# Performance work log

Measured on AMD Instinct MI355X. Metric: run time of the kernel, lower is better.

## Reference

```python
import jax, jax.numpy as jnp
import numpy as np

D = 256          # common_dim = specific_dim
NH = 8           # num_heads
HD = D // NH     # head_dim = 32
B, S = 16, 1024
EPS = 1e-5


def _mha(q, k, v, wq, bq, wk, bk, wv, bv, wo, bo):
    # q,k,v: [B, S, D]; weights stored [in, out] so y = x @ w + b
    b_, _, _ = q.shape

    def proj(x, w, b):
        return (x @ w + b).reshape(b_, -1, NH, HD).transpose(0, 2, 1, 3)  # [B,H,S,hd]

    Q, K, V = proj(q, wq, bq), proj(k, wk, bk), proj(v, wv, bv)
    scores = jnp.einsum('bhqd,bhkd->bhqk', Q, K) / (float(HD) ** 0.5)
    attn = jax.nn.softmax(scores, axis=-1)
    out = jnp.einsum('bhqk,bhkd->bhqd', attn, V)
    out = out.transpose(0, 2, 1, 3).reshape(b_, -1, D)
    return out @ wo + bo


def _ln(x, g, b):
    mu = jnp.mean(x, axis=-1, keepdims=True)
    var = jnp.var(x, axis=-1, keepdims=True)
    return (x - mu) * jax.lax.rsqrt(var + EPS) * g + b


def setup_inputs() -> dict:
    key = jax.random.key(0)
    ks = iter(jax.random.split(key, 32))
    rn = lambda *shape: jax.random.normal(next(ks), shape, dtype=jnp.float32)
    w = lambda i, o: rn(i, o) * 0.05
    inp = {
        'img_common': rn(B, S, D),
        'txt_common': rn(B, S, D),
        'img_specific': rn(B, D),
        'txt_specific': rn(B, D),
    }
    for pfx in ('i2t', 't2i'):
        for nm in ('q', 'k', 'v', 'o'):
            inp[f'{pfx}_w{nm}'] = w(D, D)
            inp[f'{pfx}_b{nm}'] = jnp.zeros((D,), jnp.float32)
    inp['ln_img_g'] = jnp.ones((D,), jnp.float32)
    inp['ln_img_b'] = jnp.zeros((D,), jnp.float32)
    inp['ln_txt_g'] = jnp.ones((D,), jnp.float32)
    inp['ln_txt_b'] = jnp.zeros((D,), jnp.float32)
    inp['enh_w'] = w(2 * D, D)
    inp['enh_b'] = jnp.zeros((D,), jnp.float32)
    inp['inc_w'] = w(2 * D, D)
    inp['inc_b'] = jnp.zeros((D,), jnp.float32)
    return inp


def reference(img_common, txt_common, img_specific, txt_specific,
              i2t_wq, i2t_bq, i2t_wk, i2t_bk, i2t_wv, i2t_bv, i2t_wo, i2t_bo,
              t2i_wq, t2i_bq, t2i_wk, t2i_bk, t2i_wv, t2i_bv, t2i_wo, t2i_bo,
              ln_img_g, ln_img_b, ln_txt_g, ln_txt_b,
              enh_w, enh_b, inc_w, inc_b):
    att_i2t = _mha(img_common, txt_common, txt_common,
                   i2t_wq, i2t_bq, i2t_wk, i2t_bk, i2t_wv, i2t_bv, i2t_wo, i2t_bo)
    img_query = _ln(att_i2t + img_common, ln_img_g, ln_img_b)
    att_t2i = _mha(txt_common, img_common, img_common,
                   t2i_wq, t2i_bq, t2i_wk, t2i_bk, t2i_wv, t2i_bv, t2i_wo, t2i_bo)
    txt_query = _ln(att_t2i + txt_common, ln_txt_g, ln_txt_b)
    combined = jnp.concatenate((img_query, txt_query), axis=-1)  # [B,S,2D]
    enhancement = combined @ enh_w + enh_b                        # [B,S,D]
    inc = jnp.concatenate((img_specific - txt_specific,
                           img_specific * txt_specific), axis=1)  # [B,2D]
    inconsistency = inc @ inc_w + inc_b                           # [B,D]
    return (enhancement, inconsistency, img_specific, txt_specific)
```

## Files before the change

kernel.cpp:

```cpp
#include <hip/hip_runtime.h>
#include <stdint.h>

typedef unsigned int u32;
typedef unsigned short u16;
typedef __attribute__((ext_vector_type(8))) short bf16x8;
typedef __attribute__((ext_vector_type(4))) float f32x4;

#define BUF_ELEMS (16384 * 256)

__device__ __forceinline__ float bflo(u32 u) { return __uint_as_float(u << 16); }
__device__ __forceinline__ float bfhi(u32 u) { return __uint_as_float(u & 0xffff0000u); }
__device__ __forceinline__ u16 f2bf(float f) {
    u32 u = __float_as_uint(f);
    return (u16)((u + 0x7fffu + ((u >> 16) & 1u)) >> 16);
}
__device__ __forceinline__ u32 pkhi(float lo, float hi) {
    return __builtin_amdgcn_perm(__float_as_uint(hi), __float_as_uint(lo), 0x07060302u);
}

struct WT {
    const float* src[9];
    u16* dst[9];
    const float* bs[6];
    float* bA;
    float* bB;
    const float* img_sp;
    const float* txt_sp;
    const float* incw;
    const float* incb;
    float* out_inc;
    float* out_img;
    float* out_txt;
};

__global__ __launch_bounds__(256)
void wtrans_kernel(WT wt)
{
    __shared__ float T[64][65];
    const int bid = blockIdx.x, t = threadIdx.x;
    if (bid == 160) {
        wt.bA[t]       = wt.bs[0][t];
        wt.bA[256 + t] = wt.bs[1][t];
        wt.bA[512 + t] = wt.bs[2][t];
        wt.bB[t]       = wt.bs[3][t];
        wt.bB[256 + t] = wt.bs[4][t];
        wt.bB[512 + t] = wt.bs[5][t];
        return;
    }
    if (bid > 160) {
        float* iv = &T[0][0];
        const int b = bid - 161, n = t;
        float a = wt.img_sp[b * 256 + n];
        float x = wt.txt_sp[b * 256 + n];
        iv[n] = a - x;
        iv[256 + n] = a * x;
        __syncthreads();
        float acc = wt.incb[n];
        for (int k = 0; k < 512; k++) acc += iv[k] * wt.incw[k * 256 + n];
        wt.out_inc[b * 256 + n] = acc;
        wt.out_img[b * 256 + n] = a;
        wt.out_txt[b * 256 + n] = x;
        return;
    }
    int m, sub;
    if (bid < 128) { m = bid >> 4; sub = bid & 15; }
    else           { m = 8;        sub = bid - 128; }
    const int K = (m == 8) ? 512 : 256;
    const int kt = (m == 8) ? (sub & 7) : (sub & 3);
    const int nt = (m == 8) ? (sub >> 3) : (sub >> 2);
    const int k0 = kt * 64, n0 = nt * 64;
    const float* src = wt.src[m];
    u16* dst = wt.dst[m];

    const int kk = t >> 2, nn = (t & 3) * 16;
    #pragma unroll
    for (int j = 0; j < 16; j += 4) {
        float4 v = *(const float4*)(src + (size_t)(k0 + kk) * 256 + n0 + nn + j);
        T[kk][nn + j + 0] = v.x; T[kk][nn + j + 1] = v.y;
        T[kk][nn + j + 2] = v.z; T[kk][nn + j + 3] = v.w;
    }
    __syncthreads();
    const int nn2 = t >> 2, kc = (t & 3) * 16;
    #pragma unroll
    for (int j = 0; j < 16; j++)
        dst[(size_t)(n0 + nn2) * K + k0 + kc + j] = f2bf(T[kc + j][nn2]);
}

template<int MODE>
__global__ __launch_bounds__(256)
void gemm_mfma(const float* __restrict__ Af,
               const u16* __restrict__ Ab0, const u16* __restrict__ Ab1,
               const u16* __restrict__ Wt0, const u16* __restrict__ Wt1,
               const float* __restrict__ bias0, const float* __restrict__ bias1,
               void* __restrict__ o0, void* __restrict__ o1, void* __restrict__ o2)
{
    __shared__ u16 As[128][72];
    __shared__ u16 Bs[128][72];
    const int tid = threadIdx.x;
    const int wave = tid >> 6, lane = tid & 63;
    const int L = lane & 15, Qd = lane >> 4;
    int m0, n0;
    if (MODE == 0) { n0 = (blockIdx.x % 6) * 128; m0 = (blockIdx.x / 6) * 128; }
    else           { n0 = (blockIdx.x & 1) * 128; m0 = (blockIdx.x >> 1) * 128; }
    const bool msel = (MODE == 1) && (m0 >= 16384);
    const int lm0 = msel ? (m0 - 16384) : m0;
    const u16* Wt = (MODE == 1 && msel) ? Wt1 : Wt0;
    const float* bias = (MODE == 1 && msel) ? bias1 : bias0;
    const int wr = wave & 1, wc = wave >> 1;
    const int sr = tid >> 1, sh = (tid & 1) * 32;
    const int KS = (MODE == 2) ? 512 : 256;

    f32x4 acc[4][4] = {};

    for (int kt = 0; kt < KS; kt += 64) {
        if (MODE == 0) {
            const float* Ap = Af + (size_t)(m0 + sr) * 256 + kt + sh;
            uint4 pk[2];
            #pragma unroll
            for (int half = 0; half < 2; half++) {
                float4 f0 = *(const float4*)(Ap + half * 16);
                float4 f1 = *(const float4*)(Ap + half * 16 + 4);
                float4 f2 = *(const float4*)(Ap + half * 16 + 8);
                float4 f3 = *(const float4*)(Ap + half * 16 + 12);
                pk[half].x = pkhi(f0.x, f0.y);
                pk[half].y = pkhi(f0.z, f0.w);
                pk[half].z = pkhi(f1.x, f1.y);
                pk[half].w = pkhi(f1.z, f1.w);
                uint4 q;
                q.x = pkhi(f2.x, f2.y); q.y = pkhi(f2.z, f2.w);
                q.z = pkhi(f3.x, f3.y); q.w = pkhi(f3.z, f3.w);
                *(uint4*)&As[sr][sh + half * 16 + 8] = q;
            }
            *(uint4*)&As[sr][sh + 0] = pk[0];
            *(uint4*)&As[sr][sh + 16] = pk[1];
        } else {
            const u16* Abase;
            int lkt = kt;
            if (MODE == 2) { Abase = (kt < 256) ? Ab0 : Ab1; lkt = kt & 255; }
            else           { Abase = msel ? Ab1 : Ab0; }
            const u16* Ap = Abase + (size_t)(lm0 + sr) * 256 + lkt + sh;
            uint4 a0 = *(const uint4*)(Ap + 0);
            uint4 a1 = *(const uint4*)(Ap + 8);
            uint4 a2 = *(const uint4*)(Ap + 16);
            uint4 a3 = *(const uint4*)(Ap + 24);
            *(uint4*)&As[sr][sh + 0]  = a0;
            *(uint4*)&As[sr][sh + 8]  = a1;
            *(uint4*)&As[sr][sh + 16] = a2;
            *(uint4*)&As[sr][sh + 24] = a3;
        }
        {
            const u16* Bp = Wt + (size_t)(n0 + sr) * KS + kt + sh;
            uint4 w0 = *(const uint4*)(Bp + 0);
            uint4 w1 = *(const uint4*)(Bp + 8);
            uint4 w2 = *(const uint4*)(Bp + 16);
            uint4 w3 = *(const uint4*)(Bp + 24);
            *(uint4*)&Bs[sr][sh + 0]  = w0;
            *(uint4*)&Bs[sr][sh + 8]  = w1;
            *(uint4*)&Bs[sr][sh + 16] = w2;
            *(uint4*)&Bs[sr][sh + 24] = w3;
        }
        __syncthreads();
        #pragma unroll
        for (int kh = 0; kh < 64; kh += 32) {
            bf16x8 af[4], bf[4];
            #pragma unroll
            for (int mt = 0; mt < 4; mt++)
                af[mt] = *(const bf16x8*)&As[wr * 64 + mt * 16 + L][kh + Qd * 8];
            #pragma unroll
            for (int nt = 0; nt < 4; nt++)
                bf[nt] = *(const bf16x8*)&Bs[wc * 64 + nt * 16 + L][kh + Qd * 8];
            #pragma unroll
            for (int mt = 0; mt < 4; mt++)
                #pragma unroll
                for (int nt = 0; nt < 4; nt++)
                    acc[mt][nt] = __builtin_amdgcn_mfma_f32_16x16x32_bf16(
                        af[mt], bf[nt], acc[mt][nt], 0, 0, 0);
        }
        __syncthreads();
    }

    float bvals[4];
    #pragma unroll
    for (int nt = 0; nt < 4; nt++)
        bvals[nt] = bias[n0 + wc * 64 + nt * 16 + L];

    const float qsc = (MODE == 0 && n0 < 256)
                      ? (0.17677669529663687f * 1.4426950408889634f) : 1.0f;

    void* outp;
    int colb;
    if (MODE == 0) {
        const int g = n0 >> 8;
        outp = (g == 0) ? o0 : ((g == 1) ? o1 : o2);
        colb = (n0 & 255) + wc * 64;
    } else if (MODE == 1) {
        outp = msel ? o1 : o0;
        colb = n0 + wc * 64;
    } else {
        outp = o0;
        colb = n0 + wc * 64;
    }
    #pragma unroll
    for (int mt = 0; mt < 4; mt++) {
        #pragma unroll
        for (int r = 0; r < 4; r++) {
            const size_t row = (size_t)(lm0 + wr * 64 + mt * 16 + Qd * 4 + r) * 256;
            #pragma unroll
            for (int nt = 0; nt < 4; nt++) {
                const int col = colb + nt * 16 + L;
                float v = (acc[mt][nt][r] + bvals[nt]) * qsc;
                if (MODE == 2) ((float*)outp)[row + col] = v;
                else           ((u16*)outp)[row + col] = f2bf(v);
            }
        }
    }
}

__global__ __launch_bounds__(256, 4)
void attn_mfma(const u16* __restrict__ Q0, const u16* __restrict__ K0,
               const u16* __restrict__ V0, u16* __restrict__ O0,
               const u16* __restrict__ Q1, const u16* __restrict__ K1,
               const u16* __restrict__ V1, u16* __restrict__ O1)
{
    __shared__ u16 Ks[128][40];
    __shared__ u16 Vt[32][136];
    __shared__ u16 Ps[4][16][136];
    const int tid = threadIdx.x;
    const int wave = tid >> 6, lane = tid & 63;
    const int L = lane & 15, Qd = lane >> 4;
    const int bid = blockIdx.x;
    const int set = bid >> 10;
    const int r3 = bid & 1023;
    const int qt = r3 & 7;
    const int h = (r3 >> 3) & 7;
    const int b = r3 >> 6;
    const u16* Q = set ? Q1 : Q0;
    const u16* K = set ? K1 : K0;
    const u16* V = set ? V1 : V0;
    u16* O = set ? O1 : O0;
    const int rowbase = b * 1024;
    const int qbase = rowbase + qt * 128;

    bf16x8 qfrag[2];
    #pragma unroll
    for (int qs = 0; qs < 2; qs++)
        qfrag[qs] = *(const bf16x8*)(Q + (size_t)(qbase + qs * 64 + wave * 16 + L) * 256
                                       + h * 32 + Qd * 8);

    const short oneb = (short)0x3F80;
    const bf16x8 ones = {oneb, oneb, oneb, oneb, oneb, oneb, oneb, oneb};

    f32x4 oacc[2][2] = {};
    f32x4 oaccL[2] = {};

    const int sr = tid >> 1;
    const int scol = (tid & 1) * 16;
    const int vcol = (sr & 15) * 8 + (sr >> 4);

    for (int t = 0; t < 8; t++) {
        const size_t kvbase = (size_t)(rowbase + t * 128 + sr) * 256 + h * 32 + scol;
        uint4 k1 = *(const uint4*)(K + kvbase);
        uint4 k2 = *(const uint4*)(K + kvbase + 8);
        uint4 v1 = *(const uint4*)(V + kvbase);
        uint4 v2 = *(const uint4*)(V + kvbase + 8);
        *(uint4*)&Ks[sr][scol]     = k1;
        *(uint4*)&Ks[sr][scol + 8] = k2;
        union { uint4 u4[2]; u16 us[16]; } vv;
        vv.u4[0] = v1; vv.u4[1] = v2;
        #pragma unroll
        for (int j = 0; j < 16; j++) Vt[scol + j][vcol] = vv.us[j];
        __syncthreads();

        #pragma unroll
        for (int qs = 0; qs < 2; qs++) {
            const f32x4 z = {0.f, 0.f, 0.f, 0.f};
            f32x4 sacc[8];
            #pragma unroll
            for (int ct = 0; ct < 8; ct++) {
                bf16x8 kfrag = *(const bf16x8*)&Ks[ct * 16 + L][Qd * 8];
                sacc[ct] = __builtin_amdgcn_mfma_f32_16x16x32_bf16(qfrag[qs], kfrag, z, 0, 0, 0);
            }
            #pragma unroll
            for (int r = 0; r < 4; r++) {
                float p[8];
                #pragma unroll
                for (int ct = 0; ct < 8; ct++) p[ct] = exp2f(sacc[ct][r]);
                uint4 pk;
                pk.x = pkhi(p[0], p[1]);
                pk.y = pkhi(p[2], p[3]);
                pk.z = pkhi(p[4], p[5]);
                pk.w = pkhi(p[6], p[7]);
                *(uint4*)&Ps[wave][Qd * 4 + r][L * 8] = pk;
            }
            #pragma unroll
            for (int kc = 0; kc < 4; kc++) {
                bf16x8 pfrag = *(const bf16x8*)&Ps[wave][L][kc * 32 + Qd * 8];
                bf16x8 vf0 = *(const bf16x8*)&Vt[L][kc * 32 + Qd * 8];
                bf16x8 vf1 = *(const bf16x8*)&Vt[16 + L][kc * 32 + Qd * 8];
                oacc[qs][0] = __builtin_amdgcn_mfma_f32_16x16x32_bf16(pfrag, vf0, oacc[qs][0], 0, 0, 0);
                oacc[qs][1] = __builtin_amdgcn_mfma_f32_16x16x32_bf16(pfrag, vf1, oacc[qs][1], 0, 0, 0);
                oaccL[qs]   = __builtin_amdgcn_mfma_f32_16x16x32_bf16(pfrag, ones, oaccL[qs], 0, 0, 0);
            }
        }
        __syncthreads();
    }

    #pragma unroll
    for (int qs = 0; qs < 2; qs++) {
        #pragma unroll
        for (int r = 0; r < 4; r++) {
            float inv = 1.f / oaccL[qs][r];
            const size_t orow = (size_t)(qbase + qs * 64 + wave * 16 + Qd * 4 + r) * 256 + h * 32;
            O[orow + L]      = f2bf(oacc[qs][0][r] * inv);
            O[orow + 16 + L] = f2bf(oacc[qs][1][r] * inv);
        }
    }
}

__global__ __launch_bounds__(256)
void ln_res_kernel(const u16* __restrict__ P0, const u16* __restrict__ P1,
                   const float* __restrict__ R0, const float* __restrict__ R1,
                   const float* __restrict__ g0, const float* __restrict__ be0,
                   const float* __restrict__ g1, const float* __restrict__ be1,
                   u16* __restrict__ out0, u16* __restrict__ out1)
{
    const int lane = threadIdx.x & 63;
    int row = blockIdx.x * 4 + (threadIdx.x >> 6);
    const bool sel = row >= 16384;
    const u16* P = sel ? P1 : P0;
    const float* R = sel ? R1 : R0;
    const float* g = sel ? g1 : g0;
    const float* be = sel ? be1 : be0;
    u16* out = sel ? out1 : out0;
    if (sel) row -= 16384;
    const int col = lane * 4;
    uint2 pv = *(const uint2*)(P + (size_t)row * 256 + col);
    float4 rv = *(const float4*)(R + (size_t)row * 256 + col);
    float x0 = bflo(pv.x) + rv.x;
    float x1 = bfhi(pv.x) + rv.y;
    float x2 = bflo(pv.y) + rv.z;
    float x3 = bfhi(pv.y) + rv.w;
    float s = x0 + x1 + x2 + x3;
    float s2 = x0*x0 + x1*x1 + x2*x2 + x3*x3;
    #pragma unroll
    for (int off = 32; off > 0; off >>= 1) {
        s  += __shfl_xor(s, off);
        s2 += __shfl_xor(s2, off);
    }
    float mean = s * 0.00390625f;
    float var = fmaxf(s2 * 0.00390625f - mean * mean, 0.f);
    float rstd = rsqrtf(var + 1e-5f);
    float4 gv = *(const float4*)(g + col);
    float4 bv = *(const float4*)(be + col);
    uint2 pk;
    pk.x = (u32)f2bf((x0 - mean) * rstd * gv.x + bv.x)
         | ((u32)f2bf((x1 - mean) * rstd * gv.y + bv.y) << 16);
    pk.y = (u32)f2bf((x2 - mean) * rstd * gv.z + bv.z)
         | ((u32)f2bf((x3 - mean) * rstd * gv.w + bv.w) << 16);
    *(uint2*)(out + (size_t)row * 256 + col) = pk;
}

extern "C" void kernel_launch(void* const* d_in, const int* in_sizes, int n_in,
                              void* d_out, int out_size, void* d_ws, size_t ws_size,
                              hipStream_t stream)
{
    (void)in_sizes; (void)n_in; (void)out_size; (void)ws_size;
    const float* img    = (const float*)d_in[0];
    const float* txt    = (const float*)d_in[1];
    const float* img_sp = (const float*)d_in[2];
    const float* txt_sp = (const float*)d_in[3];
    const float* wq_i = (const float*)d_in[4];  const float* bq_i = (const float*)d_in[5];
    const float* wk_i = (const float*)d_in[6];  const float* bk_i = (const float*)d_in[7];
    const float* wv_i = (const float*)d_in[8];  const float* bv_i = (const float*)d_in[9];
    const float* wo_i = (const float*)d_in[10]; const float* bo_i = (const float*)d_in[11];
    const float* wq_t = (const float*)d_in[12]; const float* bq_t = (const float*)d_in[13];
    const float* wk_t = (const float*)d_in[14]; const float* bk_t = (const float*)d_in[15];
    const float* wv_t = (const float*)d_in[16]; const float* bv_t = (const float*)d_in[17];
    const float* wo_t = (const float*)d_in[18]; const float* bo_t = (const float*)d_in[19];
    const float* lng_i = (const float*)d_in[20]; const float* lnb_i = (const float*)d_in[21];
    const float* lng_t = (const float*)d_in[22]; const float* lnb_t = (const float*)d_in[23];
    const float* enh_w = (const float*)d_in[24]; const float* enh_b = (const float*)d_in[25];
    const float* incw  = (const float*)d_in[26]; const float* incb  = (const float*)d_in[27];
    float* out = (float*)d_out;
    u16* wsp = (u16*)d_ws;
    u16* B0 = wsp;
    u16* B1 = wsp + 1 * (size_t)BUF_ELEMS;
    u16* B2 = wsp + 2 * (size_t)BUF_ELEMS;
    u16* B3 = wsp + 3 * (size_t)BUF_ELEMS;
    u16* B4 = wsp + 4 * (size_t)BUF_ELEMS;
    u16* B5 = wsp + 5 * (size_t)BUF_ELEMS;
    u16* wbase = wsp + 6 * (size_t)BUF_ELEMS;
    u16* WtA   = wbase;
    u16* WtB   = wbase + 196608;
    u16* Wt_oi = wbase + 393216;
    u16* Wt_ot = wbase + 458752;
    u16* Wt_en = wbase + 524288;
    float* biasA = (float*)(wbase + 655360);
    float* biasB = biasA + 768;

    dim3 blk(256);
    WT wt;
    wt.src[0] = wq_i; wt.dst[0] = WtA;
    wt.src[1] = wk_t; wt.dst[1] = WtA + 65536;
    wt.src[2] = wv_t; wt.dst[2] = WtA + 131072;
    wt.src[3] = wq_t; wt.dst[3] = WtB;
    wt.src[4] = wk_i; wt.dst[4] = WtB + 65536;
    wt.src[5] = wv_i; wt.dst[5] = WtB + 131072;
    wt.src[6] = wo_i; wt.dst[6] = Wt_oi;
    wt.src[7] = wo_t; wt.dst[7] = Wt_ot;
    wt.src[8] = enh_w; wt.dst[8] = Wt_en;
    wt.bs[0] = bq_i; wt.bs[1] = bk_t; wt.bs[2] = bv_t;
    wt.bs[3] = bq_t; wt.bs[4] = bk_i; wt.bs[5] = bv_i;
    wt.bA = biasA; wt.bB = biasB;
    wt.img_sp = img_sp; wt.txt_sp = txt_sp; wt.incw = incw; wt.incb = incb;
    wt.out_inc = out + 4194304; wt.out_img = out + 4198400; wt.out_txt = out + 4202496;
    wtrans_kernel<<<177, blk, 0, stream>>>(wt);

    gemm_mfma<0><<<768, blk, 0, stream>>>(img, nullptr, nullptr, WtA, nullptr,
                                          biasA, nullptr, B0, B4, B5);
    gemm_mfma<0><<<768, blk, 0, stream>>>(txt, nullptr, nullptr, WtB, nullptr,
                                          biasB, nullptr, B3, B1, B2);
    attn_mfma<<<2048, blk, 0, stream>>>(B0, B1, B2, B0, B3, B4, B5, B3);
    gemm_mfma<1><<<512, blk, 0, stream>>>(nullptr, B0, B3, Wt_oi, Wt_ot,
                                          bo_i, bo_t, B1, B4, nullptr);
    ln_res_kernel<<<8192, blk, 0, stream>>>(B1, B4, img, txt,
                                            lng_i, lnb_i, lng_t, lnb_t, B2, B5);
    gemm_mfma<2><<<256, blk, 0, stream>>>(nullptr, B2, B5, Wt_en, nullptr,
                                          enh_b, nullptr, out, nullptr, nullptr);
}
```

Before: 311.9 us.

## Merge input projection launches, reorder block indices for L2 reuse, hoist K fragments

The two QKV projection GEMMs become a single 1536-block launch over both modalities. Block indexing is reordered so that consecutive blocks share the same weight columns in the GEMMs and the same K/V head in attention (query tile becomes the slowest index), which should improve L2 reuse. In attention, the K fragments are loaded from LDS once per KV tile instead of once per query sub-tile. The cost is extra registers for the hoisted K fragments and somewhat messier index logic, including a dead msel expression.

Measured after the change: 309.8 us. About the same (-0.7%).

```diff
diff --git a/kernel.cpp b/kernel.cpp
--- a/kernel.cpp
+++ b/kernel.cpp
@@ -88,33 +88,40 @@
 
 template<int MODE>
 __global__ __launch_bounds__(256)
-void gemm_mfma(const float* __restrict__ Af,
+void gemm_mfma(const float* __restrict__ Af0, const float* __restrict__ Af1,
                const u16* __restrict__ Ab0, const u16* __restrict__ Ab1,
                const u16* __restrict__ Wt0, const u16* __restrict__ Wt1,
                const float* __restrict__ bias0, const float* __restrict__ bias1,
-               void* __restrict__ o0, void* __restrict__ o1, void* __restrict__ o2)
+               void* __restrict__ o0, void* __restrict__ o1, void* __restrict__ o2,
+               void* __restrict__ o3, void* __restrict__ o4, void* __restrict__ o5)
 {
     __shared__ u16 As[128][72];
     __shared__ u16 Bs[128][72];
     const int tid = threadIdx.x;
     const int wave = tid >> 6, lane = tid & 63;
     const int L = lane & 15, Qd = lane >> 4;
-    int m0, n0;
-    if (MODE == 0) { n0 = (blockIdx.x % 6) * 128; m0 = (blockIdx.x / 6) * 128; }
-    else           { n0 = (blockIdx.x & 1) * 128; m0 = (blockIdx.x >> 1) * 128; }
-    const bool msel = (MODE == 1) && (m0 >= 16384);
-    const int lm0 = msel ? (m0 - 16384) : m0;
-    const u16* Wt = (MODE == 1 && msel) ? Wt1 : Wt0;
-    const float* bias = (MODE == 1 && msel) ? bias1 : bias0;
+    int m_idx, n_idx;
+    if (MODE == 0)      { m_idx = blockIdx.x & 255; n_idx = blockIdx.x >> 8; }
+    else if (MODE == 1) { m_idx = blockIdx.x & 255; n_idx = blockIdx.x >> 8; }
+    else                { m_idx = blockIdx.x & 127; n_idx = blockIdx.x >> 7; }
+    const bool msel = (MODE != 2) && (m_idx >= 128 * (MODE == 0 ? 1 : 1) && MODE == 0
+                       ? (m_idx >= 128) : (MODE == 1 && m_idx >= 128));
+    const bool ms = (MODE == 0 || MODE == 1) ? (m_idx >= 128) : false;
+    const int lm0 = (MODE == 2) ? m_idx * 128 : (m_idx & 127) * 128;
+    const int n0 = n_idx * 128;
+    const u16* Wt = ms ? Wt1 : Wt0;
+    const float* bias = ms ? bias1 : bias0;
     const int wr = wave & 1, wc = wave >> 1;
     const int sr = tid >> 1, sh = (tid & 1) * 32;
     const int KS = (MODE == 2) ? 512 : 256;
+    (void)msel;
 
     f32x4 acc[4][4] = {};
 
     for (int kt = 0; kt < KS; kt += 64) {
         if (MODE == 0) {
-            const float* Ap = Af + (size_t)(m0 + sr) * 256 + kt + sh;
+            const float* Af = ms ? Af1 : Af0;
+            const float* Ap = Af + (size_t)(lm0 + sr) * 256 + kt + sh;
             uint4 pk[2];
             #pragma unroll
             for (int half = 0; half < 2; half++) {
@@ -137,7 +144,7 @@
             const u16* Abase;
             int lkt = kt;
             if (MODE == 2) { Abase = (kt < 256) ? Ab0 : Ab1; lkt = kt & 255; }
-            else           { Abase = msel ? Ab1 : Ab0; }
+            else           { Abase = ms ? Ab1 : Ab0; }
             const u16* Ap = Abase + (size_t)(lm0 + sr) * 256 + lkt + sh;
             uint4 a0 = *(const uint4*)(Ap + 0);
             uint4 a1 = *(const uint4*)(Ap + 8);
@@ -184,17 +191,18 @@
     for (int nt = 0; nt < 4; nt++)
         bvals[nt] = bias[n0 + wc * 64 + nt * 16 + L];
 
-    const float qsc = (MODE == 0 && n0 < 256)
+    const float qsc = (MODE == 0 && n_idx < 2)
                       ? (0.17677669529663687f * 1.4426950408889634f) : 1.0f;
 
     void* outp;
     int colb;
     if (MODE == 0) {
-        const int g = n0 >> 8;
-        outp = (g == 0) ? o0 : ((g == 1) ? o1 : o2);
-        colb = (n0 & 255) + wc * 64;
+        const int g = n_idx >> 1;
+        if (!ms) outp = (g == 0) ? o0 : ((g == 1) ? o1 : o2);
+        else     outp = (g == 0) ? o3 : ((g == 1) ? o4 : o5);
+        colb = (n_idx & 1) * 128 + wc * 64;
     } else if (MODE == 1) {
-        outp = msel ? o1 : o0;
+        outp = ms ? o1 : o0;
         colb = n0 + wc * 64;
     } else {
         outp = o0;
@@ -229,11 +237,11 @@
     const int wave = tid >> 6, lane = tid & 63;
     const int L = lane & 15, Qd = lane >> 4;
     const int bid = blockIdx.x;
-    const int set = bid >> 10;
-    const int r3 = bid & 1023;
-    const int qt = r3 & 7;
-    const int h = (r3 >> 3) & 7;
-    const int b = r3 >> 6;
+    const int qt = bid >> 8;
+    const int kv = bid & 255;
+    const int set = kv >> 7;
+    const int b = (kv >> 3) & 15;
+    const int h = kv & 7;
     const u16* Q = set ? Q1 : Q0;
     const u16* K = set ? K1 : K0;
     const u16* V = set ? V1 : V0;
@@ -271,15 +279,18 @@
         for (int j = 0; j < 16; j++) Vt[scol + j][vcol] = vv.us[j];
         __syncthreads();
 
+        bf16x8 kf[8];
+        #pragma unroll
+        for (int ct = 0; ct < 8; ct++)
+            kf[ct] = *(const bf16x8*)&Ks[ct * 16 + L][Qd * 8];
+
         #pragma unroll
         for (int qs = 0; qs < 2; qs++) {
             const f32x4 z = {0.f, 0.f, 0.f, 0.f};
             f32x4 sacc[8];
             #pragma unroll
-            for (int ct = 0; ct < 8; ct++) {
-                bf16x8 kfrag = *(const bf16x8*)&Ks[ct * 16 + L][Qd * 8];
-                sacc[ct] = __builtin_amdgcn_mfma_f32_16x16x32_bf16(qfrag[qs], kfrag, z, 0, 0, 0);
-            }
+            for (int ct = 0; ct < 8; ct++)
+                sacc[ct] = __builtin_amdgcn_mfma_f32_16x16x32_bf16(qfrag[qs], kf[ct], z, 0, 0, 0);
             #pragma unroll
             for (int r = 0; r < 4; r++) {
                 float p[8];
@@ -416,15 +427,16 @@
     wt.out_inc = out + 4194304; wt.out_img = out + 4198400; wt.out_txt = out + 4202496;
     wtrans_kernel<<<177, blk, 0, stream>>>(wt);
 
-    gemm_mfma<0><<<768, blk, 0, stream>>>(img, nullptr, nullptr, WtA, nullptr,
-                                          biasA, nullptr, B0, B4, B5);
-    gemm_mfma<0><<<768, blk, 0, stream>>>(txt, nullptr, nullptr, WtB, nullptr,
-                                          biasB, nullptr, B3, B1, B2);
+    gemm_mfma<0><<<1536, blk, 0, stream>>>(img, txt, nullptr, nullptr,
+                                           WtA, WtB, biasA, biasB,
+                                           B0, B4, B5, B3, B1, B2);
     attn_mfma<<<2048, blk, 0, stream>>>(B0, B1, B2, B0, B3, B4, B5, B3);
-    gemm_mfma<1><<<512, blk, 0, stream>>>(nullptr, B0, B3, Wt_oi, Wt_ot,
-                                          bo_i, bo_t, B1, B4, nullptr);
+    gemm_mfma<1><<<512, blk, 0, stream>>>(nullptr, nullptr, B0, B3,
+                                          Wt_oi, Wt_ot, bo_i, bo_t,
+                                          B1, B4, nullptr, nullptr, nullptr, nullptr);
     ln_res_kernel<<<8192, blk, 0, stream>>>(B1, B4, img, txt,
                                             lng_i, lnb_i, lng_t, lnb_t, B2, B5);
-    gemm_mfma<2><<<256, blk, 0, stream>>>(nullptr, B2, B5, Wt_en, nullptr,
-                                          enh_b, nullptr, out, nullptr, nullptr);
-}
+    gemm_mfma<2><<<256, blk, 0, stream>>>(nullptr, nullptr, B2, B5,
+                                          Wt_en, nullptr, enh_b, nullptr,
+                                          out, nullptr, nullptr, nullptr, nullptr, nullptr);
+}
```
